# Performance work log

Measured on AMD Instinct MI355X. Metric: run time of the kernel, lower is better.

## Reference

```python
import jax, jax.numpy as jnp
import numpy as np

E = 12      # embed dim
H = 32      # MLP hidden
EPS = 1e-5  # LayerNorm eps


def _layer_norm(x, gamma, beta):
    mu = jnp.mean(x, axis=-1, keepdims=True)
    var = jnp.mean(jnp.square(x - mu), axis=-1, keepdims=True)
    return (x - mu) * jax.lax.rsqrt(var + EPS) * gamma + beta


def setup_inputs() -> dict:
    key = jax.random.key(0)
    ks = jax.random.split(key, 16)
    L, N = 128, 4096
    s = 1.0 / np.sqrt(E)
    inp = {
        "x": jax.random.normal(ks[0], (L, N, E), dtype=jnp.float32),
        # MultiheadAttention packed in-projection [3E, E] and bias [3E]
        "in_proj_w": jax.random.uniform(ks[1], (3 * E, E), minval=-s, maxval=s, dtype=jnp.float32),
        "in_proj_b": jnp.zeros((3 * E,), dtype=jnp.float32),
        "out_w": jax.random.uniform(ks[2], (E, E), minval=-s, maxval=s, dtype=jnp.float32),
        "out_b": jnp.zeros((E,), dtype=jnp.float32),
        # MLP: Linear(12,32) Tanh Linear(32,32) Tanh Linear(32,12) Tanh
        "w1": jax.random.uniform(ks[3], (H, E), minval=-s, maxval=s, dtype=jnp.float32),
        "b1": jnp.zeros((H,), dtype=jnp.float32),
        "w2": jax.random.uniform(ks[4], (H, H), minval=-1/np.sqrt(H), maxval=1/np.sqrt(H), dtype=jnp.float32),
        "b2": jnp.zeros((H,), dtype=jnp.float32),
        "w3": jax.random.uniform(ks[5], (E, H), minval=-1/np.sqrt(H), maxval=1/np.sqrt(H), dtype=jnp.float32),
        "b3": jnp.zeros((E,), dtype=jnp.float32),
        # LayerNorm affine params
        "g1": jnp.ones((E,), dtype=jnp.float32),
        "be1": jnp.zeros((E,), dtype=jnp.float32),
        "g2": jnp.ones((E,), dtype=jnp.float32),
        "be2": jnp.zeros((E,), dtype=jnp.float32),
    }
    return inp


def reference(x, in_proj_w, in_proj_b, out_w, out_b,
              w1, b1, w2, b2, w3, b3, g1, be1, g2, be2):
    # x: [L, N, E] (seq, batch, embed) -- torch MHA default layout
    # --- single-head self-attention ---
    qkv = jnp.einsum('lne,fe->lnf', x, in_proj_w) + in_proj_b  # [L, N, 3E]
    q, k, v = jnp.split(qkv, 3, axis=-1)
    scale = 1.0 / jnp.sqrt(jnp.asarray(E, x.dtype))
    scores = jnp.einsum('lne,mne->nlm', q * scale, k)          # [N, L, L]
    p = jax.nn.softmax(scores, axis=-1)
    attn = jnp.einsum('nlm,mne->lne', p, v)                    # [L, N, E]
    attn = jnp.einsum('lne,fe->lnf', attn, out_w) + out_b
    # dropout is inactive in eval mode
    x = _layer_norm(x + attn, g1, be1)
    # --- MLP with tanh activations ---
    h = jnp.tanh(jnp.einsum('lne,he->lnh', x, w1) + b1)
    h = jnp.tanh(jnp.einsum('lnh,gh->lng', h, w2) + b2)
    ff = jnp.tanh(jnp.einsum('lnh,eh->lne', h, w3) + b3)
    x = _layer_norm(x + ff, g2, be2)
    return x
```

## Files before the change

### kernel.cpp

```cpp
#include <hip/hip_runtime.h>

#define NDIM 4096
#define LDIM 128
#define EDIM 12
#define HDIM 32
#define XPITCH 24

typedef float    f2  __attribute__((ext_vector_type(2)));
typedef float    f4v __attribute__((ext_vector_type(4)));
typedef _Float16 h2  __attribute__((ext_vector_type(2)));
typedef _Float16 h4  __attribute__((ext_vector_type(4)));

#ifndef __has_builtin
#define __has_builtin(x) 0
#endif

__device__ __forceinline__ float ex2_(float v) {
#if __has_builtin(__builtin_amdgcn_exp2f)
    return __builtin_amdgcn_exp2f(v);
#else
    return exp2f(v);
#endif
}
__device__ __forceinline__ float rcp_(float v) {
#if __has_builtin(__builtin_amdgcn_rcpf)
    return __builtin_amdgcn_rcpf(v);
#else
    return 1.0f / v;
#endif
}
__device__ __forceinline__ float rsq_(float v) {
#if __has_builtin(__builtin_amdgcn_rsqf)
    return __builtin_amdgcn_rsqf(v);
#else
    return rsqrtf(v);
#endif
}
__device__ __forceinline__ float tanh_(float v) {
    float t = ex2_(v * 2.8853900817779268f);
    return 1.0f - 2.0f * rcp_(t + 1.0f);
}

__device__ __forceinline__ h2 pk16(float a, float b) {
#if __has_builtin(__builtin_amdgcn_cvt_pkrtz)
    return __builtin_bit_cast(h2, __builtin_amdgcn_cvt_pkrtz(a, b));
#else
    h2 r; r.x = (_Float16)a; r.y = (_Float16)b; return r;
#endif
}
__device__ __forceinline__ unsigned int h2u(h2 a) { return __builtin_bit_cast(unsigned int, a); }
__device__ __forceinline__ h4 mkh4(h2 a, h2 b) {
    h4 r; r.x = a.x; r.y = a.y; r.z = b.x; r.w = b.y; return r;
}
__device__ __forceinline__ h4 cvt_h4(float4 w) { return mkh4(pk16(w.x, w.y), pk16(w.z, w.w)); }
__device__ __forceinline__ h4 h4z() {
    h4 r; r.x = (_Float16)0; r.y = (_Float16)0; r.z = (_Float16)0; r.w = (_Float16)0; return r;
}

__device__ __forceinline__ f4v mfma16(h4 a, h4 b, f4v c) {
    return __builtin_amdgcn_mfma_f32_16x16x16f16(a, b, c, 0, 0, 0);
}

__global__ __launch_bounds__(256, 3)
void encoder_fused(const float* __restrict__ x,
                   const float* __restrict__ inw, const float* __restrict__ inb,
                   const float* __restrict__ ow,  const float* __restrict__ ob,
                   const float* __restrict__ w1,  const float* __restrict__ b1,
                   const float* __restrict__ w2,  const float* __restrict__ b2,
                   const float* __restrict__ w3,  const float* __restrict__ b3,
                   const float* __restrict__ g1,  const float* __restrict__ be1,
                   const float* __restrict__ g2,  const float* __restrict__ be2,
                   float* __restrict__ out)
{
    const int tid  = threadIdx.x;
    const int p    = tid >> 7;
    const int l    = tid & 127;
    const int wv2  = (tid >> 6) & 1;
    const int lane = tid & 63;
    const int fr   = lane & 15;
    const int fg   = lane >> 4;
    const int n    = blockIdx.x * 2 + p;
    const bool e_ok = (fg < 3);

    __shared__ unsigned short sXh[2][LDIM][XPITCH];
    __shared__ unsigned short sVT[2][EDIM][132];
    __shared__ h4             sKf[2][8][64];
    __shared__ float          sMk[2][2];

    const float SCALE = 0.2886751345948129f;
    const float L2E   = 1.4426950408889634f;
    const f4v   FZ    = (f4v){0.f, 0.f, 0.f, 0.f};

    {
        const float* xp = x + ((size_t)l * NDIM + n) * EDIM;
        float4 xa = *reinterpret_cast<const float4*>(xp);
        float4 xb = *reinterpret_cast<const float4*>(xp + 4);
        float4 xc = *reinterpret_cast<const float4*>(xp + 8);
        unsigned int u0 = h2u(pk16(xa.x, xa.y)), u1 = h2u(pk16(xa.z, xa.w));
        unsigned int u2 = h2u(pk16(xb.x, xb.y)), u3 = h2u(pk16(xb.z, xb.w));
        unsigned int u4 = h2u(pk16(xc.x, xc.y)), u5 = h2u(pk16(xc.z, xc.w));
        *reinterpret_cast<uint4*>(&sXh[p][l][0]) = make_uint4(u0, u1, u2, u3);
        *reinterpret_cast<uint4*>(&sXh[p][l][8]) = make_uint4(u4, u5, 0u, 0u);
    }

    h4 WQp = h4z(), WKp = h4z(), WVp = h4z();
    if (fr < 12 && e_ok) {
        WQp = cvt_h4(*reinterpret_cast<const float4*>(inw + (     fr) * 12 + 4 * fg));
        WKp = cvt_h4(*reinterpret_cast<const float4*>(inw + (12 + fr) * 12 + 4 * fg));
        WVp = cvt_h4(*reinterpret_cast<const float4*>(inw + (24 + fr) * 12 + 4 * fg));
    }
    const float4 F4Z = make_float4(0.f, 0.f, 0.f, 0.f);
    float4 bq4 = e_ok ? *reinterpret_cast<const float4*>(inb +      4 * fg) : F4Z;
    float4 bk4 = e_ok ? *reinterpret_cast<const float4*>(inb + 12 + 4 * fg) : F4Z;
    float4 bv4 = e_ok ? *reinterpret_cast<const float4*>(inb + 24 + 4 * fg) : F4Z;

    h4 qf[4];
    float qq[4];
    float mkw = 0.f;
    #pragma unroll
    for (int st = 0; st < 4; ++st) {
        const int srow = 64 * wv2 + 16 * st;
        h4 xB = *reinterpret_cast<const h4*>(&sXh[p][srow + fr][4 * fg]);

        f4v Dq = mfma16(WQp, xB, FZ);
        float q0 = (Dq[0] + bq4.x) * SCALE, q1 = (Dq[1] + bq4.y) * SCALE;
        float q2 = (Dq[2] + bq4.z) * SCALE, q3 = (Dq[3] + bq4.w) * SCALE;
        float aq = (q0*q0 + q1*q1) + (q2*q2 + q3*q3);
        aq += __shfl_xor(aq, 16); aq += __shfl_xor(aq, 32);
        qq[st] = aq;
        qf[st] = mkh4(pk16(q0 * L2E, q1 * L2E), pk16(q2 * L2E, q3 * L2E));

        f4v Dk = mfma16(WKp, xB, FZ);
        float k0 = Dk[0] + bk4.x, k1 = Dk[1] + bk4.y;
        float k2 = Dk[2] + bk4.z, k3 = Dk[3] + bk4.w;
        float kn = (k0*k0 + k1*k1) + (k2*k2 + k3*k3);
        kn += __shfl_xor(kn, 16); kn += __shfl_xor(kn, 32);
        kn = fmaxf(kn, __shfl_xor(kn, 1));
        kn = fmaxf(kn, __shfl_xor(kn, 2));
        kn = fmaxf(kn, __shfl_xor(kn, 4));
        kn = fmaxf(kn, __shfl_xor(kn, 8));
        mkw = fmaxf(mkw, kn);
        sKf[p][4 * wv2 + st][lane] = mkh4(pk16(k0, k1), pk16(k2, k3));

        f4v Dv = mfma16(WVp, xB, FZ);
        if (e_ok) {
            sVT[p][4*fg + 0][srow + fr] = __builtin_bit_cast(unsigned short, (_Float16)(Dv[0] + bv4.x));
            sVT[p][4*fg + 1][srow + fr] = __builtin_bit_cast(unsigned short, (_Float16)(Dv[1] + bv4.y));
            sVT[p][4*fg + 2][srow + fr] = __builtin_bit_cast(unsigned short, (_Float16)(Dv[2] + bv4.z));
            sVT[p][4*fg + 3][srow + fr] = __builtin_bit_cast(unsigned short, (_Float16)(Dv[3] + bv4.w));
        }
    }
    if (lane == 0) sMk[p][wv2] = mkw;
    __syncthreads();
    const float mkmax = fmaxf(sMk[p][0], sMk[p][1]);
    float m2t[4];
    #pragma unroll
    for (int st = 0; st < 4; ++st)
        m2t[st] = sqrtf(qq[st] * mkmax) * L2E;

    f4v oc[4];
    #pragma unroll
    for (int st = 0; st < 4; ++st) oc[st] = FZ;
    float psum[4] = {0.f, 0.f, 0.f, 0.f};

    #pragma unroll
    for (int u = 0; u < 8; ++u) {
        h4 kf = sKf[p][u][lane];
        h4 vf = h4z();
        if (fr < 12)
            vf = *reinterpret_cast<const h4*>(&sVT[p][fr][16 * u + 4 * fg]);
        #pragma unroll
        for (int st = 0; st < 4; ++st) {
            f4v c = mfma16(kf, qf[st], FZ);
            float p0 = ex2_(c[0] - m2t[st]);
            float p1 = ex2_(c[1] - m2t[st]);
            float p2 = ex2_(c[2] - m2t[st]);
            float p3 = ex2_(c[3] - m2t[st]);
            psum[st] += (p0 + p1) + (p2 + p3);
            h4 paf = mkh4(pk16(p0, p1), pk16(p2, p3));
            oc[st] = mfma16(vf, paf, oc[st]);
        }
    }
    float inv[4];
    #pragma unroll
    for (int st = 0; st < 4; ++st) {
        psum[st] += __shfl_xor(psum[st], 16);
        psum[st] += __shfl_xor(psum[st], 32);
        inv[st] = rcp_(fmaxf(psum[st], 1e-35f));
    }

    h4 OWf = h4z();
    if (fr < 12 && e_ok)
        OWf = cvt_h4(*reinterpret_cast<const float4*>(ow + fr * 12 + 4 * fg));
    h4 W1f[2] = {h4z(), h4z()};
    if (e_ok) {
        W1f[0] = cvt_h4(*reinterpret_cast<const float4*>(w1 + (fr     ) * 12 + 4 * fg));
        W1f[1] = cvt_h4(*reinterpret_cast<const float4*>(w1 + (fr + 16) * 12 + 4 * fg));
    }
    h4 W2f[2][2];
    #pragma unroll
    for (int gt = 0; gt < 2; ++gt)
        #pragma unroll
        for (int ks = 0; ks < 2; ++ks)
            W2f[gt][ks] = cvt_h4(*reinterpret_cast<const float4*>(
                w2 + (16*gt + fr) * 32 + 16*ks + 4*fg));
    h4 W3f[2] = {h4z(), h4z()};
    if (fr < 12) {
        W3f[0] = cvt_h4(*reinterpret_cast<const float4*>(w3 + fr * 32 +      4 * fg));
        W3f[1] = cvt_h4(*reinterpret_cast<const float4*>(w3 + fr * 32 + 16 + 4 * fg));
    }
    float4 ob4  = e_ok ? *reinterpret_cast<const float4*>(ob  + 4*fg) : F4Z;
    float4 b3v  = e_ok ? *reinterpret_cast<const float4*>(b3  + 4*fg) : F4Z;
    float4 g1v  = e_ok ? *reinterpret_cast<const float4*>(g1  + 4*fg) : F4Z;
    float4 be1v = e_ok ? *reinterpret_cast<const float4*>(be1 + 4*fg) : F4Z;
    float4 g2v  = e_ok ? *reinterpret_cast<const float4*>(g2  + 4*fg) : F4Z;
    float4 be2v = e_ok ? *reinterpret_cast<const float4*>(be2 + 4*fg) : F4Z;
    float4 b1t0 = *reinterpret_cast<const float4*>(b1 +      4*fg);
    float4 b1t1 = *reinterpret_cast<const float4*>(b1 + 16 + 4*fg);
    float4 b2t0 = *reinterpret_cast<const float4*>(b2 +      4*fg);
    float4 b2t1 = *reinterpret_cast<const float4*>(b2 + 16 + 4*fg);

    #pragma unroll
    for (int st = 0; st < 4; ++st) {
        const int sample = 64*wv2 + 16*st + fr;
        h4 B0 = mkh4(pk16(oc[st][0]*inv[st], oc[st][1]*inv[st]),
                     pk16(oc[st][2]*inv[st], oc[st][3]*inv[st]));
        f4v D0 = mfma16(OWf, B0, FZ);
        float r0 = 0.f, r1 = 0.f, r2_ = 0.f, r3 = 0.f;
        if (e_ok) {
            h4 xh4 = *reinterpret_cast<const h4*>(&sXh[p][sample][4 * fg]);
            r0 = D0[0] + ob4.x + (float)xh4.x;
            r1 = D0[1] + ob4.y + (float)xh4.y;
            r2_= D0[2] + ob4.z + (float)xh4.z;
            r3 = D0[3] + ob4.w + (float)xh4.w;
        }
        float s = (r0 + r1) + (r2_ + r3);
        s += __shfl_xor(s, 16); s += __shfl_xor(s, 32);
        float mu = s * (1.0f / 12.0f);
        float d0 = r0 - mu, d1 = r1 - mu, d2 = r2_ - mu, d3 = r3 - mu;
        float vv = e_ok ? ((d0*d0 + d1*d1) + (d2*d2 + d3*d3)) : 0.f;
        vv += __shfl_xor(vv, 16); vv += __shfl_xor(vv, 32);
        float rs = rsq_(vv * (1.0f / 12.0f) + 1e-5f);
        float y0 = 0.f, y1 = 0.f, y2 = 0.f, y3 = 0.f;
        if (e_ok) {
            y0 = d0 * rs * g1v.x + be1v.x;
            y1 = d1 * rs * g1v.y + be1v.y;
            y2 = d2 * rs * g1v.z + be1v.z;
            y3 = d3 * rs * g1v.w + be1v.w;
        }
        h4 yB = mkh4(pk16(y0, y1), pk16(y2, y3));
        f4v D1a = mfma16(W1f[0], yB, FZ);
        f4v D1b = mfma16(W1f[1], yB, FZ);
        h4 B1a = mkh4(pk16(tanh_(D1a[0] + b1t0.x), tanh_(D1a[1] + b1t0.y)),
                      pk16(tanh_(D1a[2] + b1t0.z), tanh_(D1a[3] + b1t0.w)));
        h4 B1b = mkh4(pk16(tanh_(D1b[0] + b1t1.x), tanh_(D1b[1] + b1t1.y)),
                      pk16(tanh_(D1b[2] + b1t1.z), tanh_(D1b[3] + b1t1.w)));
        f4v D2a = mfma16(W2f[0][1], B1b, mfma16(W2f[0][0], B1a, FZ));
        f4v D2b = mfma16(W2f[1][1], B1b, mfma16(W2f[1][0], B1a, FZ));
        h4 B2a = mkh4(pk16(tanh_(D2a[0] + b2t0.x), tanh_(D2a[1] + b2t0.y)),
                      pk16(tanh_(D2a[2] + b2t0.z), tanh_(D2a[3] + b2t0.w)));
        h4 B2b = mkh4(pk16(tanh_(D2b[0] + b2t1.x), tanh_(D2b[1] + b2t1.y)),
                      pk16(tanh_(D2b[2] + b2t1.z), tanh_(D2b[3] + b2t1.w)));
        f4v D3 = mfma16(W3f[1], B2b, mfma16(W3f[0], B2a, FZ));
        float q0 = 0.f, q1 = 0.f, q2 = 0.f, q3 = 0.f;
        if (e_ok) {
            q0 = y0 + tanh_(D3[0] + b3v.x);
            q1 = y1 + tanh_(D3[1] + b3v.y);
            q2 = y2 + tanh_(D3[2] + b3v.z);
            q3 = y3 + tanh_(D3[3] + b3v.w);
        }
        float s2 = (q0 + q1) + (q2 + q3);
        s2 += __shfl_xor(s2, 16); s2 += __shfl_xor(s2, 32);
        float mu2 = s2 * (1.0f / 12.0f);
        float e0 = q0 - mu2, e1 = q1 - mu2, e2 = q2 - mu2, e3 = q3 - mu2;
        float vv2 = e_ok ? ((e0*e0 + e1*e1) + (e2*e2 + e3*e3)) : 0.f;
        vv2 += __shfl_xor(vv2, 16); vv2 += __shfl_xor(vv2, 32);
        float rs2 = rsq_(vv2 * (1.0f / 12.0f) + 1e-5f);
        if (e_ok) {
            float z0 = e0 * rs2 * g2v.x + be2v.x;
            float z1 = e1 * rs2 * g2v.y + be2v.y;
            float z2 = e2 * rs2 * g2v.z + be2v.z;
            float z3 = e3 * rs2 * g2v.w + be2v.w;
            float* op = out + ((size_t)sample * NDIM + n) * EDIM + 4 * fg;
            *reinterpret_cast<float4*>(op) = make_float4(z0, z1, z2, z3);
        }
    }
}

extern "C" void kernel_launch(void* const* d_in, const int* in_sizes, int n_in,
                              void* d_out, int out_size, void* d_ws, size_t ws_size,
                              hipStream_t stream) {
    const float* x   = (const float*)d_in[0];
    const float* inw = (const float*)d_in[1];
    const float* inb = (const float*)d_in[2];
    const float* ow  = (const float*)d_in[3];
    const float* ob  = (const float*)d_in[4];
    const float* w1  = (const float*)d_in[5];
    const float* b1  = (const float*)d_in[6];
    const float* w2  = (const float*)d_in[7];
    const float* b2  = (const float*)d_in[8];
    const float* w3  = (const float*)d_in[9];
    const float* b3  = (const float*)d_in[10];
    const float* g1  = (const float*)d_in[11];
    const float* be1 = (const float*)d_in[12];
    const float* g2  = (const float*)d_in[13];
    const float* be2 = (const float*)d_in[14];
    float* out = (float*)d_out;

    encoder_fused<<<dim3(NDIM / 2), dim3(256), 0, stream>>>(
        x, inw, inb, ow, ob, w1, b1, w2, b2, w3, b3, g1, be1, g2, be2, out);
}
```

Before: 45.41 us.

## Use one batch element per 128-thread block and reload residual in fp32

Each block now handles one batch element with 128 threads instead of two elements with 256 threads. This halves the per-block shared memory, raises the launch-bounds occupancy hint to 6 blocks, and shortens barriers to two waves. A barrier is added after the shared-memory store of x, and the residual add now re-reads x from global memory in fp32 rather than using the fp16 copy in shared memory. This improves accuracy but adds global loads, which may be served from cache.

```diff
diff --git a/kernel.cpp b/kernel.cpp
--- a/kernel.cpp
+++ b/kernel.cpp
@@ -6,7 +6,6 @@
 #define HDIM 32
 #define XPITCH 24
 
-typedef float    f2  __attribute__((ext_vector_type(2)));
 typedef float    f4v __attribute__((ext_vector_type(4)));
 typedef _Float16 h2  __attribute__((ext_vector_type(2)));
 typedef _Float16 h4  __attribute__((ext_vector_type(4)));
@@ -61,7 +60,7 @@
     return __builtin_amdgcn_mfma_f32_16x16x16f16(a, b, c, 0, 0, 0);
 }
 
-__global__ __launch_bounds__(256, 3)
+__global__ __launch_bounds__(128, 6)
 void encoder_fused(const float* __restrict__ x,
                    const float* __restrict__ inw, const float* __restrict__ inb,
                    const float* __restrict__ ow,  const float* __restrict__ ob,
@@ -73,19 +72,18 @@
                    float* __restrict__ out)
 {
     const int tid  = threadIdx.x;
-    const int p    = tid >> 7;
-    const int l    = tid & 127;
-    const int wv2  = (tid >> 6) & 1;
+    const int l    = tid;
+    const int wv2  = tid >> 6;
     const int lane = tid & 63;
     const int fr   = lane & 15;
     const int fg   = lane >> 4;
-    const int n    = blockIdx.x * 2 + p;
+    const int n    = blockIdx.x;
     const bool e_ok = (fg < 3);
 
-    __shared__ unsigned short sXh[2][LDIM][XPITCH];
-    __shared__ unsigned short sVT[2][EDIM][132];
-    __shared__ h4             sKf[2][8][64];
-    __shared__ float          sMk[2][2];
+    __shared__ unsigned short sXh[LDIM][XPITCH];
+    __shared__ unsigned short sVT[EDIM][132];
+    __shared__ h4             sKf[8][64];
+    __shared__ float          sMk[2];
 
     const float SCALE = 0.2886751345948129f;
     const float L2E   = 1.4426950408889634f;
@@ -99,8 +97,8 @@
         unsigned int u0 = h2u(pk16(xa.x, xa.y)), u1 = h2u(pk16(xa.z, xa.w));
         unsigned int u2 = h2u(pk16(xb.x, xb.y)), u3 = h2u(pk16(xb.z, xb.w));
         unsigned int u4 = h2u(pk16(xc.x, xc.y)), u5 = h2u(pk16(xc.z, xc.w));
-        *reinterpret_cast<uint4*>(&sXh[p][l][0]) = make_uint4(u0, u1, u2, u3);
-        *reinterpret_cast<uint4*>(&sXh[p][l][8]) = make_uint4(u4, u5, 0u, 0u);
+        *reinterpret_cast<uint4*>(&sXh[l][0]) = make_uint4(u0, u1, u2, u3);
+        *reinterpret_cast<uint4*>(&sXh[l][8]) = make_uint4(u4, u5, 0u, 0u);
     }
 
     h4 WQp = h4z(), WKp = h4z(), WVp = h4z();
@@ -114,13 +112,15 @@
     float4 bk4 = e_ok ? *reinterpret_cast<const float4*>(inb + 12 + 4 * fg) : F4Z;
     float4 bv4 = e_ok ? *reinterpret_cast<const float4*>(inb + 24 + 4 * fg) : F4Z;
 
+    __syncthreads();
+
     h4 qf[4];
     float qq[4];
     float mkw = 0.f;
     #pragma unroll
     for (int st = 0; st < 4; ++st) {
         const int srow = 64 * wv2 + 16 * st;
-        h4 xB = *reinterpret_cast<const h4*>(&sXh[p][srow + fr][4 * fg]);
+        h4 xB = *reinterpret_cast<const h4*>(&sXh[srow + fr][4 * fg]);
 
         f4v Dq = mfma16(WQp, xB, FZ);
         float q0 = (Dq[0] + bq4.x) * SCALE, q1 = (Dq[1] + bq4.y) * SCALE;
@@ -140,19 +140,19 @@
         kn = fmaxf(kn, __shfl_xor(kn, 4));
         kn = fmaxf(kn, __shfl_xor(kn, 8));
         mkw = fmaxf(mkw, kn);
-        sKf[p][4 * wv2 + st][lane] = mkh4(pk16(k0, k1), pk16(k2, k3));
+        sKf[4 * wv2 + st][lane] = mkh4(pk16(k0, k1), pk16(k2, k3));
 
         f4v Dv = mfma16(WVp, xB, FZ);
         if (e_ok) {
-            sVT[p][4*fg + 0][srow + fr] = __builtin_bit_cast(unsigned short, (_Float16)(Dv[0] + bv4.x));
-            sVT[p][4*fg + 1][srow + fr] = __builtin_bit_cast(unsigned short, (_Float16)(Dv[1] + bv4.y));
-            sVT[p][4*fg + 2][srow + fr] = __builtin_bit_cast(unsigned short, (_Float16)(Dv[2] + bv4.z));
-            sVT[p][4*fg + 3][srow + fr] = __builtin_bit_cast(unsigned short, (_Float16)(Dv[3] + bv4.w));
-        }
-    }
-    if (lane == 0) sMk[p][wv2] = mkw;
+            sVT[4*fg + 0][srow + fr] = __builtin_bit_cast(unsigned short, (_Float16)(Dv[0] + bv4.x));
+            sVT[4*fg + 1][srow + fr] = __builtin_bit_cast(unsigned short, (_Float16)(Dv[1] + bv4.y));
+            sVT[4*fg + 2][srow + fr] = __builtin_bit_cast(unsigned short, (_Float16)(Dv[2] + bv4.z));
+            sVT[4*fg + 3][srow + fr] = __builtin_bit_cast(unsigned short, (_Float16)(Dv[3] + bv4.w));
+        }
+    }
+    if (lane == 0) sMk[wv2] = mkw;
     __syncthreads();
-    const float mkmax = fmaxf(sMk[p][0], sMk[p][1]);
+    const float mkmax = fmaxf(sMk[0], sMk[1]);
     float m2t[4];
     #pragma unroll
     for (int st = 0; st < 4; ++st)
@@ -165,10 +165,10 @@
 
     #pragma unroll
     for (int u = 0; u < 8; ++u) {
-        h4 kf = sKf[p][u][lane];
+        h4 kf = sKf[u][lane];
         h4 vf = h4z();
         if (fr < 12)
-            vf = *reinterpret_cast<const h4*>(&sVT[p][fr][16 * u + 4 * fg]);
+            vf = *reinterpret_cast<const h4*>(&sVT[fr][16 * u + 4 * fg]);
         #pragma unroll
         for (int st = 0; st < 4; ++st) {
             f4v c = mfma16(kf, qf[st], FZ);
@@ -228,11 +228,12 @@
         f4v D0 = mfma16(OWf, B0, FZ);
         float r0 = 0.f, r1 = 0.f, r2_ = 0.f, r3 = 0.f;
         if (e_ok) {
-            h4 xh4 = *reinterpret_cast<const h4*>(&sXh[p][sample][4 * fg]);
-            r0 = D0[0] + ob4.x + (float)xh4.x;
-            r1 = D0[1] + ob4.y + (float)xh4.y;
-            r2_= D0[2] + ob4.z + (float)xh4.z;
-            r3 = D0[3] + ob4.w + (float)xh4.w;
+            float4 xres = *reinterpret_cast<const float4*>(
+                x + ((size_t)sample * NDIM + n) * EDIM + 4 * fg);
+            r0 = D0[0] + ob4.x + xres.x;
+            r1 = D0[1] + ob4.y + xres.y;
+            r2_= D0[2] + ob4.z + xres.z;
+            r3 = D0[3] + ob4.w + xres.w;
         }
         float s = (r0 + r1) + (r2_ + r3);
         s += __shfl_xor(s, 16); s += __shfl_xor(s, 32);
@@ -307,6 +308,6 @@
     const float* be2 = (const float*)d_in[14];
     float* out = (float*)d_out;
 
-    encoder_fused<<<dim3(NDIM / 2), dim3(256), 0, stream>>>(
+    encoder_fused<<<dim3(NDIM), dim3(LDIM), 0, stream>>>(
         x, inw, inb, ow, ob, w1, b1, w2, b2, w3, b3, g1, be1, g2, be2, out);
 }
```

Result: slower. 126.7 us (+179.1%).
